# Performance work log

Hardware: AMD Instinct MI355X
Metric: run time of the kernel (lower is better)

Reference implementation:

```python
import jax, jax.numpy as jnp
import numpy as np

B, SQ, SK, D, H = 4, 2048, 2048, 1024, 16
HD = D // H


def setup_inputs() -> dict:
    key = jax.random.key(0)
    ks = jax.random.split(key, 12)
    s = 1.0 / np.sqrt(D)
    return {
        "query": jax.random.normal(ks[0], (B, SQ, D), jnp.float32),
        "key": jax.random.normal(ks[1], (B, SK, D), jnp.float32),
        "value": jax.random.normal(ks[2], (B, SK, D), jnp.float32),
        "key_padding_mask": jax.random.randint(ks[3], (B, SK), 0, 2, jnp.int32),
        "Wq": jax.random.uniform(ks[4], (D, D), jnp.float32, -s, s),
        "bq": jnp.zeros((D,), jnp.float32),
        "Wk": jax.random.uniform(ks[5], (D, D), jnp.float32, -s, s),
        "bk": jnp.zeros((D,), jnp.float32),
        "Wv": jax.random.uniform(ks[6], (D, D), jnp.float32, -s, s),
        "bv": jnp.zeros((D,), jnp.float32),
        "Wo": jax.random.uniform(ks[7], (D, D), jnp.float32, -s, s),
        "bo": jnp.zeros((D,), jnp.float32),
    }


def reference(query, key, value, key_padding_mask, Wq, bq, Wk, bk, Wv, bv, Wo, bo):
    scale = HD ** -0.5
    # projections: torch Linear is x @ W.T + b
    q = (query @ Wq.T + bq).reshape(B, SQ, H, HD).transpose(0, 2, 1, 3)  # [B,H,SQ,HD]
    k = (key @ Wk.T + bk).reshape(B, SK, H, HD).transpose(0, 2, 1, 3)    # [B,H,SK,HD]
    v = (value @ Wv.T + bv).reshape(B, SK, H, HD).transpose(0, 2, 1, 3)  # [B,H,SK,HD]
    scores = jnp.einsum("bhqd,bhkd->bhqk", q, k) * scale                  # [B,H,SQ,SK]
    mask = key_padding_mask[:, None, None, :] != 0                        # True = keep
    scores = jnp.where(mask, scores, -jnp.inf)
    attn = jax.nn.softmax(scores, axis=-1)
    # dropout is identity at inference (eval mode)
    out = jnp.einsum("bhqk,bhkd->bhqd", attn, v)                          # [B,H,SQ,HD]
    out = out.transpose(0, 2, 1, 3).reshape(B, SQ, D)
    return out @ Wo.T + bo
```

## Files before the change

kernel.cpp:

```cpp
#include <hip/hip_runtime.h>


typedef __bf16 bf16_t;
typedef __attribute__((ext_vector_type(4))) __bf16 bf16x4;
typedef __attribute__((ext_vector_type(8))) __bf16 bf16x8;
typedef __attribute__((ext_vector_type(4))) float f32x4;

#define MFMA16(a, b, c) __builtin_amdgcn_mfma_f32_16x16x32_bf16(a, b, c, 0, 0, 0)

#define WAITV(N) asm volatile("s_waitcnt vmcnt(" #N ")" ::: "memory")

__device__ __forceinline__ void gl_lds16(const void* g, void* l) {
  __builtin_amdgcn_global_load_lds(
      (const __attribute__((address_space(1))) unsigned int*)g,
      (__attribute__((address_space(3))) unsigned int*)l, 16, 0, 0);
}

__device__ __forceinline__ void block_barrier() {
  asm volatile("" ::: "memory");
  __builtin_amdgcn_s_barrier();
  asm volatile("" ::: "memory");
}

__global__ void conv_kernel(const float* __restrict__ q, const float* __restrict__ k,
                            const float* __restrict__ v, const float* __restrict__ Wq,
                            const float* __restrict__ Wk, const float* __restrict__ Wv,
                            const float* __restrict__ Wo, bf16_t* __restrict__ q16,
                            bf16_t* __restrict__ k16, bf16_t* __restrict__ v16,
                            bf16_t* __restrict__ W16) {
  const int y = blockIdx.y;
  const float* src;
  bf16_t* dst;
  size_t idx;
  if (y < 3) {
    src = (y == 0) ? q : (y == 1) ? k : v;
    dst = (y == 0) ? q16 : (y == 1) ? k16 : v16;
    idx = ((size_t)blockIdx.x * 256 + threadIdx.x) * 4;
  } else {
    if (blockIdx.x >= 4096) return;
    const int m = blockIdx.x >> 10;
    src = (m == 0) ? Wq : (m == 1) ? Wk : (m == 2) ? Wv : Wo;
    dst = W16 + ((size_t)m << 20);
    idx = (((size_t)(blockIdx.x & 1023)) * 256 + threadIdx.x) * 4;
  }
  float4 w = *(const float4*)(src + idx);
  bf16x4 pk;
  pk[0] = (bf16_t)w.x; pk[1] = (bf16_t)w.y; pk[2] = (bf16_t)w.z; pk[3] = (bf16_t)w.w;
  *(bf16x4*)(dst + idx) = pk;
}

__global__ void addp_kernel(float* __restrict__ dst, const float* __restrict__ src) {
  const size_t idx = ((size_t)blockIdx.x * 256 + threadIdx.x) * 4;
  float4 a = *(const float4*)(dst + idx);
  float4 b = *(const float4*)(src + idx);
  a.x += b.x; a.y += b.y; a.z += b.z; a.w += b.w;
  *(float4*)(dst + idx) = a;
}

template <int NSTEP>
__global__ __launch_bounds__(256, 2) void gemm_kernel(
    const bf16_t* __restrict__ A0, const bf16_t* __restrict__ A1,
    const bf16_t* __restrict__ A2, const bf16_t* __restrict__ W0,
    const bf16_t* __restrict__ W1, const bf16_t* __restrict__ W2,
    const float* __restrict__ b0, const float* __restrict__ b1,
    const float* __restrict__ b2, void* __restrict__ o0, void* __restrict__ o1,
    void* __restrict__ o2, const int md0, const int md1, const int md2,
    const int kb0, const int kb1, const int kb2) {
  __shared__ __align__(16) bf16_t As[2][16 * 512];
  __shared__ __align__(16) bf16_t Bs[2][16 * 512];

  const int z = blockIdx.z;
  const bf16_t* A = (z == 0) ? A0 : (z == 1) ? A1 : A2;
  const bf16_t* Bw = (z == 0) ? W0 : (z == 1) ? W1 : W2;
  const float* bias = (z == 0) ? b0 : (z == 1) ? b1 : b2;
  void* outp = (z == 0) ? o0 : (z == 1) ? o1 : o2;
  const int out_mode = (z == 0) ? md0 : (z == 1) ? md1 : md2;
  const int kbase = (z == 0) ? kb0 : (z == 1) ? kb1 : kb2;

  const int tid = threadIdx.x;
  const int lane = tid & 63, wave = tid >> 6;
  const int fm = lane & 15, quad = lane >> 4;
  const int wr = wave >> 1, wc = wave & 1;
  const int m0 = blockIdx.x * 128, n0 = blockIdx.y * 128;

  f32x4 acc[4][4];
#pragma unroll
  for (int i = 0; i < 4; ++i)
#pragma unroll
    for (int j = 0; j < 4; ++j) acc[i][j] = f32x4{0.f, 0.f, 0.f, 0.f};

  auto stage = [&](int ks, int buf) {
    const int k0 = kbase + ks * 64;
#pragma unroll
    for (int it = 0; it < 4; ++it) {
      const int fid = wave * 4 + it;
      const int row = (fid >> 1) * 16 + fm;
      const int col = (fid & 1) * 32 + quad * 8;
      gl_lds16(A + (size_t)(m0 + row) * 1024 + k0 + col, As[buf] + fid * 512);
    }
#pragma unroll
    for (int it = 0; it < 4; ++it) {
      const int fid = wave * 4 + it;
      const int row = (fid >> 1) * 16 + fm;
      const int col = (fid & 1) * 32 + quad * 8;
      gl_lds16(Bw + (size_t)(n0 + row) * 1024 + k0 + col, Bs[buf] + fid * 512);
    }
  };

  stage(0, 0);
  for (int ks = 0; ks < NSTEP; ++ks) {
    if (ks + 1 < NSTEP) {
      stage(ks + 1, (ks + 1) & 1);
      WAITV(8);
    } else {
      WAITV(0);
    }
    block_barrier();
    const bf16_t* Ab = As[ks & 1];
    const bf16_t* Bb = Bs[ks & 1];
#pragma unroll
    for (int u = 0; u < 2; ++u) {
      bf16x8 af[4], bfr[4];
#pragma unroll
      for (int i = 0; i < 4; ++i)
        af[i] = *(const bf16x8*)(Ab + ((4 * wr + i) * 2 + u) * 512 + lane * 8);
#pragma unroll
      for (int j = 0; j < 4; ++j)
        bfr[j] = *(const bf16x8*)(Bb + ((4 * wc + j) * 2 + u) * 512 + lane * 8);
#pragma unroll
      for (int i = 0; i < 4; ++i)
#pragma unroll
        for (int j = 0; j < 4; ++j) acc[i][j] = MFMA16(af[i], bfr[j], acc[i][j]);
    }
    block_barrier();
  }

  float bval[4];
#pragma unroll
  for (int j = 0; j < 4; ++j)
    bval[j] = bias ? bias[n0 + wc * 64 + j * 16 + fm] : 0.0f;

#pragma unroll
  for (int i = 0; i < 4; ++i) {
#pragma unroll
    for (int j = 0; j < 4; ++j) {
      const int col = n0 + wc * 64 + j * 16 + fm;
#pragma unroll
      for (int r = 0; r < 4; ++r) {
        const int row = m0 + wr * 64 + i * 16 + quad * 4 + r;
        const float v = acc[i][j][r] + bval[j];
        if (out_mode == 2) {
          ((float*)outp)[(size_t)row * 1024 + col] = v;
        } else if (out_mode == 0) {
          ((bf16_t*)outp)[(size_t)row * 1024 + col] = (bf16_t)v;
        } else {
          const int bb = row >> 11, sk = row & 2047;
          const int tt = sk >> 7, L128 = sk & 127;
          const int c = L128 >> 5, hf = (L128 >> 4) & 1;
          const int qd = (L128 >> 2) & 3, rr = L128 & 3;
          const int hh = col >> 6, hd = col & 63;
          const int nt = hd >> 4, fv = hd & 15;
          const size_t idx = (((size_t)(bb * 16 + hh)) << 17) + tt * 8192 +
                             (nt * 4 + c) * 512 + (qd * 16 + fv) * 8 + hf * 4 + rr;
          ((bf16_t*)outp)[idx] = (bf16_t)v;
        }
      }
    }
  }
}

__global__ __launch_bounds__(256, 2) void attn_kernel(
    const bf16_t* __restrict__ q16, const bf16_t* __restrict__ k16,
    const bf16_t* __restrict__ vt16, const int* __restrict__ mask,
    bf16_t* __restrict__ o16) {
  __shared__ __align__(16) bf16_t Kb[2][8192];
  __shared__ __align__(16) bf16_t Vb[2][8192];
  __shared__ float mbuf[2][128];
  __shared__ float lbuf[128];

  const int tid = threadIdx.x;
  const int lane = tid & 63, wave = tid >> 6;
  const int fm = lane & 15, quad = lane >> 4;
  const int lin = blockIdx.y * 16 + blockIdx.x;
  const int xcd = lin & 7, slot = lin >> 3;
  const int qt = slot & 15;
  const int bh = ((slot >> 4) << 3) + xcd;
  const int b = bh >> 4, h = bh & 15;
  const float SC = 0.125f * 1.44269504f;

  bf16x8 aq[2][2];
#pragma unroll
  for (int i = 0; i < 2; ++i)
#pragma unroll
    for (int dc = 0; dc < 2; ++dc) {
      const int row = qt * 128 + (2 * wave + i) * 16 + fm;
      aq[i][dc] = *(const bf16x8*)(q16 + ((size_t)(b * 2048 + row)) * 1024 + h * 64 +
                                   dc * 32 + quad * 8);
    }

  auto stageKV = [&](int t, int buf) {
    const bf16_t* kb = k16 + ((size_t)(b * 2048 + t * 128)) * 1024 + h * 64;
#pragma unroll
    for (int s = 0; s < 4; ++s) {
      const int fid = wave * 4 + s;
      const int row = (fid >> 1) * 16 + fm;
      const int col = (fid & 1) * 32 + quad * 8;
      gl_lds16(kb + (size_t)row * 1024 + col, Kb[buf] + fid * 512);
    }
    const bf16_t* vbase = vt16 + ((size_t)bh << 17) + t * 8192;
#pragma unroll
    for (int s = 0; s < 4; ++s) {
      const int fid = wave * 4 + s;
      gl_lds16(vbase + fid * 512 + lane * 8, Vb[buf] + fid * 512);
    }
    if (tid < 128) mbuf[buf][tid] = mask[b * 2048 + t * 128 + tid] ? 0.0f : -1e30f;
  };

  f32x4 oacc[2][4];
#pragma unroll
  for (int i = 0; i < 2; ++i)
#pragma unroll
    for (int n = 0; n < 4; ++n) oacc[i][n] = f32x4{0.f, 0.f, 0.f, 0.f};
  float lrow[2] = {0.f, 0.f};

  stageKV(0, 0);
  for (int t = 0; t < 16; ++t) {
    __syncthreads();
    if (t + 1 < 16) stageKV(t + 1, (t + 1) & 1);
    const bf16_t* K = Kb[t & 1];
    const bf16_t* V = Vb[t & 1];
    const float* mb = mbuf[t & 1];

    f32x4 sacc[2][8];
#pragma unroll
    for (int i = 0; i < 2; ++i)
#pragma unroll
      for (int j = 0; j < 8; ++j) sacc[i][j] = f32x4{0.f, 0.f, 0.f, 0.f};
#pragma unroll
    for (int j = 0; j < 8; ++j) {
#pragma unroll
      for (int dc = 0; dc < 2; ++dc) {
        bf16x8 kf = *(const bf16x8*)(K + (j * 2 + dc) * 512 + lane * 8);
        sacc[0][j] = MFMA16(kf, aq[0][dc], sacc[0][j]);
        sacc[1][j] = MFMA16(kf, aq[1][dc], sacc[1][j]);
      }
    }

#pragma unroll
    for (int j = 0; j < 8; ++j) {
      f32x4 md = *(const f32x4*)&mb[j * 16 + quad * 4];
#pragma unroll
      for (int i = 0; i < 2; ++i) {
#pragma unroll
        for (int r = 0; r < 4; ++r) {
          const float p = __builtin_amdgcn_exp2f(fmaf(sacc[i][j][r], SC, md[r]));
          sacc[i][j][r] = p;
          lrow[i] += p;
        }
      }
    }

#pragma unroll
    for (int c = 0; c < 4; ++c) {
      bf16x8 pf[2];
#pragma unroll
      for (int i = 0; i < 2; ++i) {
#pragma unroll
        for (int r = 0; r < 4; ++r) {
          pf[i][r] = (bf16_t)sacc[i][2 * c][r];
          pf[i][4 + r] = (bf16_t)sacc[i][2 * c + 1][r];
        }
      }
#pragma unroll
      for (int n = 0; n < 4; ++n) {
        bf16x8 vv = *(const bf16x8*)(V + (n * 4 + c) * 512 + lane * 8);
        oacc[0][n] = MFMA16(pf[0], vv, oacc[0][n]);
        oacc[1][n] = MFMA16(pf[1], vv, oacc[1][n]);
      }
    }
  }

#pragma unroll
  for (int i = 0; i < 2; ++i) {
    float l = lrow[i];
    l += __shfl_xor(l, 16);
    l += __shfl_xor(l, 32);
    if (quad == 0) lbuf[wave * 32 + i * 16 + fm] = l;
  }
  __syncthreads();
#pragma unroll
  for (int i = 0; i < 2; ++i) {
    f32x4 lv = *(const f32x4*)&lbuf[wave * 32 + i * 16 + quad * 4];
#pragma unroll
    for (int r = 0; r < 4; ++r) {
      const float inv = 1.0f / lv[r];
      const int row = qt * 128 + wave * 32 + i * 16 + quad * 4 + r;
#pragma unroll
      for (int n = 0; n < 4; ++n) {
        o16[((size_t)(b * 2048 + row)) * 1024 + h * 64 + n * 16 + fm] =
            (bf16_t)(oacc[i][n][r] * inv);
      }
    }
  }
}

extern "C" void kernel_launch(void* const* d_in, const int* in_sizes, int n_in,
                              void* d_out, int out_size, void* d_ws, size_t ws_size,
                              hipStream_t stream) {
  const float* query = (const float*)d_in[0];
  const float* key   = (const float*)d_in[1];
  const float* value = (const float*)d_in[2];
  const int* mask    = (const int*)d_in[3];
  const float* Wq = (const float*)d_in[4];
  const float* bq = (const float*)d_in[5];
  const float* Wk = (const float*)d_in[6];
  const float* bk = (const float*)d_in[7];
  const float* Wv = (const float*)d_in[8];
  const float* bv = (const float*)d_in[9];
  const float* Wo = (const float*)d_in[10];
  const float* bo = (const float*)d_in[11];

  const size_t MB = 1024 * 1024;
  char* ws = (char*)d_ws;
  bf16_t* W16 = (bf16_t*)ws;
  bf16_t* qin = (bf16_t*)(ws + 8 * MB);
  bf16_t* kin = (bf16_t*)(ws + 24 * MB);
  bf16_t* vin = (bf16_t*)(ws + 40 * MB);
  bf16_t* q16 = (bf16_t*)(ws + 56 * MB);

  bf16_t* k16  = (bf16_t*)d_out;
  bf16_t* vt16 = (bf16_t*)((char*)d_out + 16 * MB);
  bf16_t* o16  = qin;
  float*  pw   = (float*)(ws + 24 * MB);

  conv_kernel<<<dim3(8192, 4), 256, 0, stream>>>(query, key, value, Wq, Wk, Wv, Wo,
                                                 qin, kin, vin, W16);

  gemm_kernel<16><<<dim3(64, 8, 3), 256, 0, stream>>>(
      qin, kin, vin, W16, W16 + 1048576, W16 + 2097152, bq, bk, bv,
      q16, k16, vt16, 0, 0, 1, 0, 0, 0);

  attn_kernel<<<dim3(16, 64), 256, 0, stream>>>(q16, k16, vt16, mask, o16);

  gemm_kernel<8><<<dim3(64, 8, 2), 256, 0, stream>>>(
      o16, o16, nullptr, W16 + 3145728, W16 + 3145728, nullptr, bo, nullptr,
      nullptr, d_out, pw, nullptr, 2, 2, 0, 0, 512, 0);

  addp_kernel<<<8192, 256, 0, stream>>>((float*)d_out, pw);
}
```

Baseline: 408.4 us.

## Enlarge GEMM tiles to 256x256 with 8 waves and interleaved prefetch

Replaces the 128x128, 4-wave projection GEMM with a 256x256, 8-wave version. It also spreads the next-tile global-to-LDS loads across four sub-steps of the MFMA loop and raises wave priority around the MFMA bursts. The goal is more operand reuse per LDS byte and better overlap of loads with math. The cost is 128KB of LDS per block and more accumulator registers, so occupancy may drop, and the grid shrinks to 384 or 256 blocks, which may fill the CUs unevenly.

```diff
diff --git a/kernel.cpp b/kernel.cpp
--- a/kernel.cpp
+++ b/kernel.cpp
@@ -57,8 +57,8 @@
   *(float4*)(dst + idx) = a;
 }
 
-template <int NSTEP>
-__global__ __launch_bounds__(256, 2) void gemm_kernel(
+template <int NK>
+__global__ __launch_bounds__(512, 2) void gemm256_kernel(
     const bf16_t* __restrict__ A0, const bf16_t* __restrict__ A1,
     const bf16_t* __restrict__ A2, const bf16_t* __restrict__ W0,
     const bf16_t* __restrict__ W1, const bf16_t* __restrict__ W2,
@@ -66,8 +66,8 @@
     const float* __restrict__ b2, void* __restrict__ o0, void* __restrict__ o1,
     void* __restrict__ o2, const int md0, const int md1, const int md2,
     const int kb0, const int kb1, const int kb2) {
-  __shared__ __align__(16) bf16_t As[2][16 * 512];
-  __shared__ __align__(16) bf16_t Bs[2][16 * 512];
+  __shared__ __align__(16) bf16_t AsL[2][32 * 512];
+  __shared__ __align__(16) bf16_t BsL[2][32 * 512];
 
   const int z = blockIdx.z;
   const bf16_t* A = (z == 0) ? A0 : (z == 1) ? A1 : A2;
@@ -80,59 +80,74 @@
   const int tid = threadIdx.x;
   const int lane = tid & 63, wave = tid >> 6;
   const int fm = lane & 15, quad = lane >> 4;
-  const int wr = wave >> 1, wc = wave & 1;
-  const int m0 = blockIdx.x * 128, n0 = blockIdx.y * 128;
-
-  f32x4 acc[4][4];
-#pragma unroll
-  for (int i = 0; i < 4; ++i)
+  const int wr = wave >> 2, wc = wave & 3;
+  const int m0 = blockIdx.x * 256, n0 = blockIdx.y * 256;
+
+  f32x4 acc[8][4];
+#pragma unroll
+  for (int i = 0; i < 8; ++i)
 #pragma unroll
     for (int j = 0; j < 4; ++j) acc[i][j] = f32x4{0.f, 0.f, 0.f, 0.f};
 
-  auto stage = [&](int ks, int buf) {
-    const int k0 = kbase + ks * 64;
-#pragma unroll
-    for (int it = 0; it < 4; ++it) {
-      const int fid = wave * 4 + it;
-      const int row = (fid >> 1) * 16 + fm;
-      const int col = (fid & 1) * 32 + quad * 8;
-      gl_lds16(A + (size_t)(m0 + row) * 1024 + k0 + col, As[buf] + fid * 512);
-    }
-#pragma unroll
-    for (int it = 0; it < 4; ++it) {
-      const int fid = wave * 4 + it;
-      const int row = (fid >> 1) * 16 + fm;
-      const int col = (fid & 1) * 32 + quad * 8;
-      gl_lds16(Bw + (size_t)(n0 + row) * 1024 + k0 + col, Bs[buf] + fid * 512);
-    }
+  auto stageA = [&](int fid, int kt, int d) {
+    const int row = m0 + (fid >> 1) * 16 + fm;
+    const int col = kbase + kt * 64 + (fid & 1) * 32 + quad * 8;
+    gl_lds16(A + (size_t)row * 1024 + col, AsL[d] + fid * 512);
   };
-
-  stage(0, 0);
-  for (int ks = 0; ks < NSTEP; ++ks) {
-    if (ks + 1 < NSTEP) {
-      stage(ks + 1, (ks + 1) & 1);
-      WAITV(8);
-    } else {
-      WAITV(0);
-    }
-    block_barrier();
-    const bf16_t* Ab = As[ks & 1];
-    const bf16_t* Bb = Bs[ks & 1];
-#pragma unroll
-    for (int u = 0; u < 2; ++u) {
-      bf16x8 af[4], bfr[4];
-#pragma unroll
-      for (int i = 0; i < 4; ++i)
-        af[i] = *(const bf16x8*)(Ab + ((4 * wr + i) * 2 + u) * 512 + lane * 8);
-#pragma unroll
-      for (int j = 0; j < 4; ++j)
-        bfr[j] = *(const bf16x8*)(Bb + ((4 * wc + j) * 2 + u) * 512 + lane * 8);
-#pragma unroll
-      for (int i = 0; i < 4; ++i)
-#pragma unroll
-        for (int j = 0; j < 4; ++j) acc[i][j] = MFMA16(af[i], bfr[j], acc[i][j]);
-    }
-    block_barrier();
+  auto stageB = [&](int fid, int kt, int d) {
+    const int row = n0 + (fid >> 1) * 16 + fm;
+    const int col = kbase + kt * 64 + (fid & 1) * 32 + quad * 8;
+    gl_lds16(Bw + (size_t)row * 1024 + col, BsL[d] + fid * 512);
+  };
+
+#pragma unroll
+  for (int it = 0; it < 4; ++it) stageA(wave * 4 + it, 0, 0);
+#pragma unroll
+  for (int it = 0; it < 4; ++it) stageB(wave * 4 + it, 0, 0);
+
+  for (int g = 0; g < NK; ++g) {
+    const int s = g & 1, d = s ^ 1;
+    const bf16_t* Ab = AsL[s];
+    const bf16_t* Bb = BsL[s];
+    bf16x8 bfv[4][2];
+#pragma unroll
+    for (int q = 0; q < 4; ++q) {
+      if (q == 0) WAITV(0);
+      block_barrier();
+      if (q == 0) {
+#pragma unroll
+        for (int j = 0; j < 4; ++j)
+#pragma unroll
+          for (int kh = 0; kh < 2; ++kh)
+            bfv[j][kh] =
+                *(const bf16x8*)(Bb + (((wc * 4 + j) << 1) + kh) * 512 + lane * 8);
+      }
+      bf16x8 af[2][2];
+#pragma unroll
+      for (int i2 = 0; i2 < 2; ++i2)
+#pragma unroll
+        for (int kh = 0; kh < 2; ++kh)
+          af[i2][kh] = *(const bf16x8*)(
+              Ab + (((wr * 8 + q * 2 + i2) << 1) + kh) * 512 + lane * 8);
+      if (g + 1 < NK) {
+        if (q < 2) {
+          stageA(wave * 4 + q * 2, g + 1, d);
+          stageA(wave * 4 + q * 2 + 1, g + 1, d);
+        } else {
+          stageB(wave * 4 + (q - 2) * 2, g + 1, d);
+          stageB(wave * 4 + (q - 2) * 2 + 1, g + 1, d);
+        }
+      }
+      __builtin_amdgcn_s_setprio(1);
+#pragma unroll
+      for (int i2 = 0; i2 < 2; ++i2)
+#pragma unroll
+        for (int j = 0; j < 4; ++j) {
+          acc[q * 2 + i2][j] = MFMA16(af[i2][0], bfv[j][0], acc[q * 2 + i2][j]);
+          acc[q * 2 + i2][j] = MFMA16(af[i2][1], bfv[j][1], acc[q * 2 + i2][j]);
+        }
+      __builtin_amdgcn_s_setprio(0);
+    }
   }
 
   float bval[4];
@@ -141,13 +156,13 @@
     bval[j] = bias ? bias[n0 + wc * 64 + j * 16 + fm] : 0.0f;
 
 #pragma unroll
-  for (int i = 0; i < 4; ++i) {
+  for (int i = 0; i < 8; ++i) {
 #pragma unroll
     for (int j = 0; j < 4; ++j) {
       const int col = n0 + wc * 64 + j * 16 + fm;
 #pragma unroll
       for (int r = 0; r < 4; ++r) {
-        const int row = m0 + wr * 64 + i * 16 + quad * 4 + r;
+        const int row = m0 + wr * 128 + i * 16 + quad * 4 + r;
         const float v = acc[i][j][r] + bval[j];
         if (out_mode == 2) {
           ((float*)outp)[(size_t)row * 1024 + col] = v;
@@ -336,13 +351,13 @@
   conv_kernel<<<dim3(8192, 4), 256, 0, stream>>>(query, key, value, Wq, Wk, Wv, Wo,
                                                  qin, kin, vin, W16);
 
-  gemm_kernel<16><<<dim3(64, 8, 3), 256, 0, stream>>>(
+  gemm256_kernel<16><<<dim3(32, 4, 3), 512, 0, stream>>>(
       qin, kin, vin, W16, W16 + 1048576, W16 + 2097152, bq, bk, bv,
       q16, k16, vt16, 0, 0, 1, 0, 0, 0);
 
   attn_kernel<<<dim3(16, 64), 256, 0, stream>>>(q16, k16, vt16, mask, o16);
 
-  gemm_kernel<8><<<dim3(64, 8, 2), 256, 0, stream>>>(
+  gemm256_kernel<8><<<dim3(32, 4, 2), 512, 0, stream>>>(
       o16, o16, nullptr, W16 + 3145728, W16 + 3145728, nullptr, bo, nullptr,
       nullptr, d_out, pw, nullptr, 2, 2, 0, 0, 512, 0);
 
```

New measurement: 407.7 us. About the same (-0.2%).
